# Kernel optimization log

Measured on AMD Instinct MI355X. Metric: run time of the kernel, lower is better.

## Reference

```python
import jax, jax.numpy as jnp
import numpy as np

FS = 512.0
N_PHA = 10
N_AMP = 10
FIR_LEN = 513  # odd, ~1 s at fs=512 -> resolves 2 Hz band edges
N_BINS = 18    # hard-coded in PAC.__init__
TEMP = 0.01    # ModulationIndex temperature (near-hard soft binning)
EPS = 1e-8


def _design_filters():
    # Windowed-sinc FIR bandpass, one kernel per band: h = lp(hi) - lp(lo), Hamming window.
    t = np.arange(FIR_LEN) - (FIR_LEN - 1) / 2.0
    win = np.hamming(FIR_LEN)
    def bp(lo, hi):
        lp = lambda fc: 2.0 * fc / FS * np.sinc(2.0 * fc / FS * t)
        return (lp(hi) - lp(lo)) * win
    pha_c = np.linspace(2.0, 20.0, N_PHA)
    amp_c = np.linspace(60.0, 160.0, N_AMP)
    bands = [(0.75 * c, 1.25 * c) for c in pha_c] + [(0.75 * c, 1.25 * c) for c in amp_c]
    return np.stack([bp(lo, hi) for lo, hi in bands]).astype(np.float32)  # (20, L)


def setup_inputs() -> dict:
    key = jax.random.key(0)
    x = jax.random.normal(key, (4, 16, 4096), dtype=jnp.float32)  # (B, C, T)
    filters = jnp.asarray(_design_filters())                      # (n_pha+n_amp, L)
    return {"x": x, "filters": filters}


def _analytic(sig):
    # FFT-based Hilbert analytic signal along last axis.
    T = sig.shape[-1]
    h = np.zeros(T, np.float32)
    h[0] = 1.0
    if T % 2 == 0:
        h[T // 2] = 1.0
        h[1:T // 2] = 2.0
    else:
        h[1:(T + 1) // 2] = 2.0
    return jnp.fft.ifft(jnp.fft.fft(sig, axis=-1) * jnp.asarray(h), axis=-1)


def reference(x, filters):
    B, C, T = x.shape
    L = filters.shape[-1]
    # Bandpass: (B*C, 1, T) x (n_bands, 1, L) -> (B*C, n_bands, T); symmetric kernels so corr == conv.
    xf = jax.lax.conv_general_dilated(
        x.reshape(-1, 1, T), filters[:, None, :],
        window_strides=(1,), padding=[(L // 2, L // 2)])
    xf = xf.reshape(B, C, -1, T)
    phase = jnp.angle(_analytic(xf[:, :, :N_PHA]))        # (B, C, P, T)
    amplitude = jnp.abs(_analytic(xf[:, :, N_PHA:]))      # (B, C, A, T)
    # Soft circular phase binning (temperature -> near one-hot).
    centers = jnp.asarray((-np.pi + 2.0 * np.pi * (np.arange(N_BINS) + 0.5) / N_BINS).astype(np.float32))
    d = jnp.mod(phase[..., None] - centers + np.pi, 2.0 * np.pi) - np.pi  # (B,C,P,T,K)
    w = jax.nn.softmax(-(d * d) / TEMP, axis=-1)
    # Mean amplitude per phase bin, per (pha, amp) band pair.
    amp_sum = jnp.einsum('bcptk,bcat->bcpak', w, amplitude)  # (B,C,P,A,K)
    cnt = w.sum(axis=-2)                                      # (B,C,P,K)
    mean_amp = amp_sum / (cnt[:, :, :, None, :] + EPS)
    p = mean_amp / (mean_amp.sum(-1, keepdims=True) + EPS)
    log_k = jnp.log(jnp.float32(N_BINS))
    mi = (log_k + (p * jnp.log(p + EPS)).sum(-1)) / log_k    # Tort MI, (B,C,P,A)
    return mi
```

## Files before the change

kernel.cpp:

```cpp
#include <hip/hip_runtime.h>
#include <math.h>

#define T_LEN 4096
#define FIR_L 513
#define N_PHA 10
#define N_AMP 10
#define N_BANDS 20
#define N_BINS 18
#define BC 64

typedef __attribute__((ext_vector_type(8))) short short8;
typedef __attribute__((ext_vector_type(4))) float f32x4;

#define ZA(i) (((i) << 1) + ((((i) >> 4)) << 1))

__device__ float2 twg_dev[1024];

static __device__ __forceinline__ unsigned short f2bf(float x) {
    unsigned u = __float_as_uint(x);
    unsigned r = u + 0x7FFFu + ((u >> 16) & 1u);
    return (unsigned short)(r >> 16);
}

static __device__ __forceinline__ int digitrev12(int p) {
    unsigned rr = __brev((unsigned)p) >> 20;
    rr = ((rr & 0x555u) << 1) | ((rr & 0xAAAu) >> 1);
    return (int)rr;
}

static __device__ __forceinline__ void tw_derive(const float2* tw, int m1,
        float& c1, float& s1, float& c2, float& s2, float& c3, float& s3) {
    const float2 w1 = tw[m1];
    c1 = w1.x; s1 = w1.y;
    s2 = 2.0f * s1 * c1;
    c2 = fmaf(-2.0f * s1, s1, 1.0f);
    c3 = c1 * c2 - s1 * s2;
    s3 = s1 * c2 + c1 * s2;
}

static __device__ __forceinline__ float2 cmul_em(float2 u, float c, float s) {
    return make_float2(u.x * c + u.y * s, u.y * c - u.x * s);
}

static __device__ __forceinline__ void bf_fwd(float2& A, float2& B, float2& C, float2& D,
        float c1, float s1, float c2, float s2, float c3, float s3) {
    const float t0r = A.x + C.x, t0i = A.y + C.y;
    const float t1r = A.x - C.x, t1i = A.y - C.y;
    const float t2r = B.x + D.x, t2i = B.y + D.y;
    const float t3r = B.x - D.x, t3i = B.y - D.y;
    const float y0r = t0r + t2r,  y0i = t0i + t2i;
    const float u1r = t1r + t3i, u1i = t1i - t3r;
    const float u2r = t0r - t2r, u2i = t0i - t2i;
    const float u3r = t1r - t3i, u3i = t1i + t3r;
    A = make_float2(y0r, y0i);
    B = make_float2(u1r * c1 + u1i * s1, u1i * c1 - u1r * s1);
    C = make_float2(u2r * c2 + u2i * s2, u2i * c2 - u2r * s2);
    D = make_float2(u3r * c3 + u3i * s3, u3i * c3 - u3r * s3);
}

static __device__ __forceinline__ void bf_inv(float2& A, float2& B, float2& C, float2& D,
        float c1, float s1, float c2, float s2, float c3, float s3) {
    const float tbr = B.x * c1 - B.y * s1, tbi = B.y * c1 + B.x * s1;
    const float tcr = C.x * c2 - C.y * s2, tci = C.y * c2 + C.x * s2;
    const float tdr = D.x * c3 - D.y * s3, tdi = D.y * c3 + D.x * s3;
    const float ar = A.x, ai = A.y;
    A = make_float2(ar + tbr + tcr + tdr, ai + tbi + tci + tdi);
    B = make_float2(ar - tbi - tcr + tdi, ai + tbr - tci - tdr);
    C = make_float2(ar - tbr + tcr - tdr, ai - tbi + tci - tdi);
    D = make_float2(ar + tbi - tcr - tdi, ai - tbr - tci + tdr);
}

static __device__ __forceinline__ void fft_fwd_passes(float* z, const float2* tw,
                                                      int tid, int s0) {
    for (int s = s0; s < 6; s += 2) {
        const int hl = 10 - 2 * s;
        const int h  = 1 << hl;
        const int h4 = h >> 2;
        const int kk = tid & (h4 - 1);
        const int g  = tid >> (hl - 2);
        const int i0 = (g << (hl + 2)) + kk;
        float2 e[4][4];
#pragma unroll
        for (int j = 0; j < 4; ++j)
#pragma unroll
            for (int r = 0; r < 4; ++r)
                e[j][r] = *(const float2*)&z[ZA(i0 + j * h4 + r * h)];
#pragma unroll
        for (int j = 0; j < 4; ++j) {
            float c1, s1, c2, s2, c3, s3;
            tw_derive(tw, (kk + j * h4) << (2 * s), c1, s1, c2, s2, c3, s3);
            bf_fwd(e[j][0], e[j][1], e[j][2], e[j][3], c1, s1, c2, s2, c3, s3);
        }
        {
            float c1, s1, c2, s2, c3, s3;
            tw_derive(tw, kk << (2 * s + 2), c1, s1, c2, s2, c3, s3);
#pragma unroll
            for (int r = 0; r < 4; ++r)
                bf_fwd(e[0][r], e[1][r], e[2][r], e[3][r], c1, s1, c2, s2, c3, s3);
        }
#pragma unroll
        for (int j = 0; j < 4; ++j)
#pragma unroll
            for (int r = 0; r < 4; ++r)
                *(float2*)&z[ZA(i0 + j * h4 + r * h)] = e[j][r];
        __syncthreads();
    }
}

static __device__ __forceinline__ void fft_fwd_pass1_sparse(
        float* z, const float2* tw, int tid, float2 F, float2 Tl) {
    float c1, s1, c2, s2, c3, s3;
    tw_derive(tw, tid, c1, s1, c2, s2, c3, s3);
    float2 P[4];
    P[0] = F;
    P[1] = cmul_em(F, c1, s1);
    P[2] = cmul_em(F, c2, s2);
    P[3] = cmul_em(F, c3, s3);
    tw_derive(tw, tid + 768, c1, s1, c2, s2, c3, s3);
    const float2 iT  = make_float2(-Tl.y,  Tl.x);
    const float2 nT  = make_float2(-Tl.x, -Tl.y);
    const float2 niT = make_float2( Tl.y, -Tl.x);
    float2 Q[4];
    Q[0] = Tl;
    Q[1] = cmul_em(iT,  c1, s1);
    Q[2] = cmul_em(nT,  c2, s2);
    Q[3] = cmul_em(niT, c3, s3);
    tw_derive(tw, tid << 2, c1, s1, c2, s2, c3, s3);
#pragma unroll
    for (int r = 0; r < 4; ++r) {
        const int ib = tid + (r << 10);
        const float2 A = make_float2(P[r].x + Q[r].x, P[r].y + Q[r].y);
        const float2 B = cmul_em(make_float2(P[r].x - Q[r].y, P[r].y + Q[r].x), c1, s1);
        const float2 C = cmul_em(make_float2(P[r].x - Q[r].x, P[r].y - Q[r].y), c2, s2);
        const float2 D = cmul_em(make_float2(P[r].x + Q[r].y, P[r].y - Q[r].x), c3, s3);
        *(float2*)&z[ZA(ib)]        = A;
        *(float2*)&z[ZA(ib + 256)]  = B;
        *(float2*)&z[ZA(ib + 512)]  = C;
        *(float2*)&z[ZA(ib + 768)]  = D;
    }
}

static __device__ __forceinline__ void fft_inv6(float* z, const float2* tw, int tid) {
#pragma unroll
    for (int s = 0; s < 6; s += 2) {
        const int L  = 1 << (2 * s);
        const int k  = tid & (L - 1);
        const int g  = tid >> (2 * s);
        const int i0 = (g << (2 * s + 4)) + k;
        float2 e[4][4];
#pragma unroll
        for (int j = 0; j < 4; ++j)
#pragma unroll
            for (int r = 0; r < 4; ++r)
                e[j][r] = *(const float2*)&z[ZA(i0 + j * L + (r << (2 * s + 2)))];
        {
            float c1, s1, c2, s2, c3, s3;
            tw_derive(tw, k << (10 - 2 * s), c1, s1, c2, s2, c3, s3);
#pragma unroll
            for (int r = 0; r < 4; ++r)
                bf_inv(e[0][r], e[1][r], e[2][r], e[3][r], c1, s1, c2, s2, c3, s3);
        }
#pragma unroll
        for (int j = 0; j < 4; ++j) {
            float c1, s1, c2, s2, c3, s3;
            tw_derive(tw, (k + j * L) << (8 - 2 * s), c1, s1, c2, s2, c3, s3);
            bf_inv(e[j][0], e[j][1], e[j][2], e[j][3], c1, s1, c2, s2, c3, s3);
        }
#pragma unroll
        for (int j = 0; j < 4; ++j)
#pragma unroll
            for (int r = 0; r < 4; ++r)
                *(float2*)&z[ZA(i0 + j * L + (r << (2 * s + 2)))] = e[j][r];
        __syncthreads();
    }
}

__global__ __launch_bounds__(256) void spectral_pre(
    const float* __restrict__ x,
    const float* __restrict__ filt,
    float2* __restrict__ Xs,
    float2* __restrict__ Hs)
{
    __shared__ float z[8704];
    __shared__ float2 twl[1024];
    __shared__ float fb[FIR_L];

    const int tid = threadIdx.x;
    const int b   = blockIdx.x;

    if (b == BC + N_BANDS) {
        for (int m = tid; m < 1024; m += 256) {
            float ang = (float)m * (6.283185307179586f / 4096.0f);
            float s, c;
            sincosf(ang, &s, &c);
            twg_dev[m] = make_float2(c, s);
        }
        return;
    }

    for (int m = tid; m < 1024; m += 256) {
        float ang = (float)m * (6.283185307179586f / 4096.0f);
        float s, c;
        sincosf(ang, &s, &c);
        twl[m] = make_float2(c, s);
    }

    if (b < BC) {
        const float* xrow = x + b * T_LEN;
        for (int i = tid; i < 4096; i += 256)
            *(float2*)&z[ZA(i)] = make_float2(xrow[i], 0.0f);
    } else {
        const int band = b - BC;
        for (int i = tid; i < FIR_L; i += 256) fb[i] = filt[band * FIR_L + i];
        __syncthreads();
        for (int i = tid; i < 4096; i += 256) {
            float hv = 0.0f;
            if (i < 257)        hv = fb[256 - i];
            else if (i >= 3840) hv = fb[4352 - i];
            *(float2*)&z[ZA(i)] = make_float2(hv, 0.0f);
        }
    }
    __syncthreads();

    fft_fwd_passes(z, twl, tid, 0);

    float2* dst = (b < BC) ? (Xs + b * 4096) : (Hs + (b - BC) * 4096);
    for (int i = tid; i < 4096; i += 256)
        dst[i] = *(const float2*)&z[ZA(i)];
}

__global__ __launch_bounds__(256, 4) void spectral_main(
    const float* __restrict__ x,
    const float* __restrict__ filt,
    const float2* __restrict__ Xs,
    const float2* __restrict__ Hs,
    float* __restrict__ pha,
    unsigned short* __restrict__ amp_bf)
{
    __shared__ float z[8704];
    __shared__ float xe[512];
    __shared__ float fb[FIR_L];

    const int tid  = threadIdx.x;
    const int bc   = blockIdx.x / N_BANDS;
    const int band = blockIdx.x % N_BANDS;
    const float2* tw = twg_dev;

    const float* xrow = x + bc * T_LEN;
    for (int i = tid; i < 512; i += 256)
        xe[i] = (i < 256) ? xrow[i] : xrow[3584 + i];
    for (int i = tid; i < FIR_L; i += 256) fb[i] = filt[band * FIR_L + i];
    __syncthreads();

    float cf = 0.0f, ct = 0.0f;
    for (int l = 0; l <= 255 - tid; ++l)
        cf = fmaf(fb[l], xe[256 + tid + l], cf);
    for (int j = 0; j <= tid; ++j)
        ct = fmaf(fb[512 - tid + j], xe[j], ct);

    fft_fwd_pass1_sparse(z, tw, tid, make_float2(-cf, 0.0f), make_float2(-ct, 0.0f));
    __syncthreads();
    fft_fwd_passes(z, tw, tid, 2);

    const float2* Xrow = Xs + bc * 4096;
    const float2* Hrow = Hs + band * 4096;
    for (int i = tid; i < 4096; i += 256) {
        const float2 X = Xrow[i];
        const float2 H = Hrow[i];
        const float2 C = *(const float2*)&z[ZA(i)];
        float pr = X.x * H.x - X.y * H.y + C.x;
        float pi = X.x * H.y + X.y * H.x + C.y;
        const int f = digitrev12(i);
        const float mf = (f == 0 || f == 2048) ? 1.0f : (f < 2048 ? 2.0f : 0.0f);
        *(float2*)&z[ZA(i)] = make_float2(pr * mf, pi * mf);
    }
    __syncthreads();

    fft_inv6(z, tw, tid);

    const float inv_n = 1.0f / 4096.0f;
    if (band < N_PHA) {
        float* dst = pha + (bc * N_PHA + band) * T_LEN;
        for (int i = tid; i < 4096; i += 256) {
            const float2 zz = *(const float2*)&z[ZA(i)];
            dst[i] = atan2f(zz.y, zz.x);
        }
    } else {
        unsigned short* dst = amp_bf + (bc * N_AMP + (band - N_PHA)) * T_LEN;
        for (int i = tid; i < 4096; i += 256) {
            const float2 zz = *(const float2*)&z[ZA(i)];
            dst[i] = f2bf(sqrtf(zz.x * zz.x + zz.y * zz.y) * inv_n);
        }
    }
}

__global__ __launch_bounds__(512) void bin_mi_mfma(
    const float* __restrict__ pha,
    const unsigned short* __restrict__ amp_bf,
    float* __restrict__ out)
{
    const int tid  = threadIdx.x;
    const int lane = tid & 63;
    const int wv   = tid >> 6;
    const int bc   = blockIdx.x / N_PHA;
    const int p    = blockIdx.x % N_PHA;

    __shared__ unsigned int wbufW[8][18 * 68];
    __shared__ float psum[8][11][N_BINS];
    __shared__ float asum[11][N_BINS];

    const float* phrow = pha + (bc * N_PHA + p) * T_LEN;
    const unsigned short* arow = amp_bf + bc * N_AMP * T_LEN;

    const float PI_F  = 3.14159274101257324f;
    const float INVD  = 2.8647889756541160f;
    const float DELTA = 0.34906585039886590f;
    const float C1    = 12.184696791468343f;
    const float C2    = 69.813170079773180f;

    const int m_ = lane & 15;
    const int q_ = lane >> 4;
    const int n_ = lane & 15;

    short8 zero8;
#pragma unroll
    for (int j = 0; j < 8; ++j) zero8[j] = 0;
    short8 ones8;
#pragma unroll
    for (int j = 0; j < 8; ++j) ones8[j] = (short)0x3F80;

    f32x4 acc0 = {0.f, 0.f, 0.f, 0.f};
    f32x4 acc1 = {0.f, 0.f, 0.f, 0.f};

    const int base_t = wv * 512;
    unsigned short* wh = (unsigned short*)&wbufW[wv][0];

    float2 pp[4];
#pragma unroll
    for (int c = 0; c < 4; ++c)
        pp[c] = *(const float2*)&phrow[base_t + c * 128 + lane * 2];

    for (int chunk = 0; chunk < 4; ++chunk) {
        const int cb = base_t + chunk * 128;

        short8 af[4];
#pragma unroll
        for (int s = 0; s < 4; ++s) {
            const int tA = cb + s * 32 + q_ * 8;
            if (m_ < N_AMP)       af[s] = *(const short8*)(arow + m_ * T_LEN + tA);
            else if (m_ == N_AMP) af[s] = ones8;
            else                  af[s] = zero8;
        }

#pragma unroll
        for (int k = 0; k < N_BINS; ++k)
            wbufW[wv][k * 68 + lane] = 0u;

#pragma unroll
        for (int h = 0; h < 2; ++h) {
            const float ph = h ? pp[chunk].y : pp[chunk].x;
            float u  = (ph + PI_F) * INVD;
            float jf = floorf(u);
            float d  = (u - jf - 0.5f) * DELTA;
            int j0 = (int)jf;
            if (j0 >= N_BINS) j0 -= N_BINS;
            const int jm = (j0 == 0) ? N_BINS - 1 : j0 - 1;
            const int jp = (j0 == N_BINS - 1) ? 0 : j0 + 1;
            const float em = expf(-C1 - C2 * d);
            const float ep = expf(-C1 + C2 * d);
            const float inv = 1.0f / (1.0f + em + ep);
            wh[(j0 * 68 + lane) * 2 + h] = f2bf(inv);
            wh[(jm * 68 + lane) * 2 + h] = f2bf(em * inv);
            wh[(jp * 68 + lane) * 2 + h] = f2bf(ep * inv);
        }
        __builtin_amdgcn_wave_barrier();

#pragma unroll
        for (int s = 0; s < 4; ++s) {
            const int woff = s * 16 + q_ * 4;
            short8 bfrag0 = *(const short8*)&wbufW[wv][n_ * 68 + woff];
            short8 bfrag1 = (n_ < 2)
                ? *(const short8*)&wbufW[wv][(16 + n_) * 68 + woff]
                : zero8;
            acc0 = __builtin_amdgcn_mfma_f32_16x16x32_bf16(af[s], bfrag0, acc0, 0, 0, 0);
            acc1 = __builtin_amdgcn_mfma_f32_16x16x32_bf16(af[s], bfrag1, acc1, 0, 0, 0);
        }
        __builtin_amdgcn_wave_barrier();
    }

#pragma unroll
    for (int r = 0; r < 4; ++r) {
        const int m = q_ * 4 + r;
        if (m < 11) {
            psum[wv][m][n_] = acc0[r];
            if (n_ < 2) psum[wv][m][16 + n_] = acc1[r];
        }
    }
    __syncthreads();

    if (tid < 11 * N_BINS) {
        const int m = tid / N_BINS;
        const int k = tid % N_BINS;
        float s = 0.0f;
#pragma unroll
        for (int w = 0; w < 8; ++w) s += psum[w][m][k];
        asum[m][k] = s;
    }
    __syncthreads();

    if (tid < N_AMP) {
        float ma[N_BINS];
        float msum = 0.0f;
#pragma unroll
        for (int k = 0; k < N_BINS; ++k) {
            float m = asum[tid][k] / (asum[10][k] + 1e-8f);
            ma[k] = m;
            msum += m;
        }
        const float inv = 1.0f / (msum + 1e-8f);
        float acc = 0.0f;
#pragma unroll
        for (int k = 0; k < N_BINS; ++k) {
            float pk = ma[k] * inv;
            acc = fmaf(pk, logf(pk + 1e-8f), acc);
        }
        const float logk = 2.89037175789124f;
        out[(bc * N_PHA + p) * N_AMP + tid] = (logk + acc) / logk;
    }
}

extern "C" void kernel_launch(void* const* d_in, const int* in_sizes, int n_in,
                              void* d_out, int out_size, void* d_ws, size_t ws_size,
                              hipStream_t stream) {
    const float* x    = (const float*)d_in[0];
    const float* filt = (const float*)d_in[1];
    float* out = (float*)d_out;

    float* pha = (float*)d_ws;
    unsigned short* amp_bf = (unsigned short*)(pha + BC * N_PHA * T_LEN);
    float2* Xs = (float2*)(amp_bf + BC * N_AMP * T_LEN);
    float2* Hs = Xs + BC * 4096;

    spectral_pre <<<BC + N_BANDS + 1, 256, 0, stream>>>(x, filt, Xs, Hs);
    spectral_main<<<BC * N_BANDS, 256, 0, stream>>>(x, filt, Xs, Hs, pha, amp_bf);
    bin_mi_mfma  <<<BC * N_PHA,   512, 0, stream>>>(pha, amp_bf, out);
}
```

Baseline: 118.2 us.

## Fuse three kernels into one cooperative persistent kernel with grid syncs

Merges the pre-FFT, spectral main and binning kernels into a single cooperative kernel that loops over work units and separates stages with grid-wide syncs. This removes two kernel launches and their gaps. To fit, the binning stage now runs with 256 threads, so each wave covers twice as many time samples, and the pre stage reads twiddles from global memory instead of a per-block table. The risks are grid sync overhead, a grid capped by occupancy, and less parallelism in the binning stage. Twiddles are written by some blocks and read by others within the same stage before the first grid sync, which may be a race.

```diff
diff --git a/kernel.cpp b/kernel.cpp
--- a/kernel.cpp
+++ b/kernel.cpp
@@ -1,5 +1,8 @@
 #include <hip/hip_runtime.h>
+#include <hip/hip_cooperative_groups.h>
 #include <math.h>
+
+namespace cg = cooperative_groups;
 
 #define T_LEN 4096
 #define FIR_L 513
@@ -175,42 +178,22 @@
     }
 }
 
-__global__ __launch_bounds__(256) void spectral_pre(
-    const float* __restrict__ x,
-    const float* __restrict__ filt,
-    float2* __restrict__ Xs,
-    float2* __restrict__ Hs)
+static __device__ void process_pre_unit(int u,
+        const float* __restrict__ x, const float* __restrict__ filt,
+        float2* __restrict__ Xs, float2* __restrict__ Hs,
+        float* smem_f, int tid)
 {
-    __shared__ float z[8704];
-    __shared__ float2 twl[1024];
-    __shared__ float fb[FIR_L];
-
-    const int tid = threadIdx.x;
-    const int b   = blockIdx.x;
-
-    if (b == BC + N_BANDS) {
-        for (int m = tid; m < 1024; m += 256) {
-            float ang = (float)m * (6.283185307179586f / 4096.0f);
-            float s, c;
-            sincosf(ang, &s, &c);
-            twg_dev[m] = make_float2(c, s);
-        }
-        return;
-    }
-
-    for (int m = tid; m < 1024; m += 256) {
-        float ang = (float)m * (6.283185307179586f / 4096.0f);
-        float s, c;
-        sincosf(ang, &s, &c);
-        twl[m] = make_float2(c, s);
-    }
-
-    if (b < BC) {
-        const float* xrow = x + b * T_LEN;
+    float* z  = smem_f;
+    float* fb = smem_f + 8704;
+
+    __syncthreads();
+
+    if (u < BC) {
+        const float* xrow = x + u * T_LEN;
         for (int i = tid; i < 4096; i += 256)
             *(float2*)&z[ZA(i)] = make_float2(xrow[i], 0.0f);
     } else {
-        const int band = b - BC;
+        const int band = u - BC;
         for (int i = tid; i < FIR_L; i += 256) fb[i] = filt[band * FIR_L + i];
         __syncthreads();
         for (int i = tid; i < 4096; i += 256) {
@@ -222,28 +205,24 @@
     }
     __syncthreads();
 
-    fft_fwd_passes(z, twl, tid, 0);
-
-    float2* dst = (b < BC) ? (Xs + b * 4096) : (Hs + (b - BC) * 4096);
+    fft_fwd_passes(z, twg_dev, tid, 0);
+
+    float2* dst = (u < BC) ? (Xs + u * 4096) : (Hs + (u - BC) * 4096);
     for (int i = tid; i < 4096; i += 256)
         dst[i] = *(const float2*)&z[ZA(i)];
 }
 
-__global__ __launch_bounds__(256, 4) void spectral_main(
-    const float* __restrict__ x,
-    const float* __restrict__ filt,
-    const float2* __restrict__ Xs,
-    const float2* __restrict__ Hs,
-    float* __restrict__ pha,
-    unsigned short* __restrict__ amp_bf)
+static __device__ void process_main_unit(int u,
+        const float* __restrict__ x, const float* __restrict__ filt,
+        const float2* __restrict__ Xs, const float2* __restrict__ Hs,
+        float* __restrict__ pha, unsigned short* __restrict__ amp_bf,
+        float* smem_f, int tid)
 {
-    __shared__ float z[8704];
-    __shared__ float xe[512];
-    __shared__ float fb[FIR_L];
-
-    const int tid  = threadIdx.x;
-    const int bc   = blockIdx.x / N_BANDS;
-    const int band = blockIdx.x % N_BANDS;
+    float* z  = smem_f;
+    float* xe = smem_f + 8704;
+    float* fb = smem_f + 9216;
+    const int bc   = u / N_BANDS;
+    const int band = u % N_BANDS;
     const float2* tw = twg_dev;
 
     const float* xrow = x + bc * T_LEN;
@@ -294,20 +273,18 @@
     }
 }
 
-__global__ __launch_bounds__(512) void bin_mi_mfma(
-    const float* __restrict__ pha,
-    const unsigned short* __restrict__ amp_bf,
-    float* __restrict__ out)
+static __device__ void process_bin_unit(int unit,
+        const float* __restrict__ pha, const unsigned short* __restrict__ amp_bf,
+        float* __restrict__ out, float* smem_f, int tid)
 {
-    const int tid  = threadIdx.x;
+    unsigned int* wbuf = (unsigned int*)smem_f;
+    float* psum = smem_f + 4896;
+    float* asum = smem_f + 5688;
+
     const int lane = tid & 63;
     const int wv   = tid >> 6;
-    const int bc   = blockIdx.x / N_PHA;
-    const int p    = blockIdx.x % N_PHA;
-
-    __shared__ unsigned int wbufW[8][18 * 68];
-    __shared__ float psum[8][11][N_BINS];
-    __shared__ float asum[11][N_BINS];
+    const int bc   = unit / N_PHA;
+    const int p    = unit % N_PHA;
 
     const float* phrow = pha + (bc * N_PHA + p) * T_LEN;
     const unsigned short* arow = amp_bf + bc * N_AMP * T_LEN;
@@ -332,15 +309,16 @@
     f32x4 acc0 = {0.f, 0.f, 0.f, 0.f};
     f32x4 acc1 = {0.f, 0.f, 0.f, 0.f};
 
-    const int base_t = wv * 512;
-    unsigned short* wh = (unsigned short*)&wbufW[wv][0];
-
-    float2 pp[4];
-#pragma unroll
-    for (int c = 0; c < 4; ++c)
+    const int base_t = wv * 1024;
+    unsigned int* wrow = wbuf + wv * 1224;
+    unsigned short* wh = (unsigned short*)wrow;
+
+    float2 pp[8];
+#pragma unroll
+    for (int c = 0; c < 8; ++c)
         pp[c] = *(const float2*)&phrow[base_t + c * 128 + lane * 2];
 
-    for (int chunk = 0; chunk < 4; ++chunk) {
+    for (int chunk = 0; chunk < 8; ++chunk) {
         const int cb = base_t + chunk * 128;
 
         short8 af[4];
@@ -354,7 +332,7 @@
 
 #pragma unroll
         for (int k = 0; k < N_BINS; ++k)
-            wbufW[wv][k * 68 + lane] = 0u;
+            wrow[k * 68 + lane] = 0u;
 
 #pragma unroll
         for (int h = 0; h < 2; ++h) {
@@ -378,9 +356,9 @@
 #pragma unroll
         for (int s = 0; s < 4; ++s) {
             const int woff = s * 16 + q_ * 4;
-            short8 bfrag0 = *(const short8*)&wbufW[wv][n_ * 68 + woff];
+            short8 bfrag0 = *(const short8*)&wrow[n_ * 68 + woff];
             short8 bfrag1 = (n_ < 2)
-                ? *(const short8*)&wbufW[wv][(16 + n_) * 68 + woff]
+                ? *(const short8*)&wrow[(16 + n_) * 68 + woff]
                 : zero8;
             acc0 = __builtin_amdgcn_mfma_f32_16x16x32_bf16(af[s], bfrag0, acc0, 0, 0, 0);
             acc1 = __builtin_amdgcn_mfma_f32_16x16x32_bf16(af[s], bfrag1, acc1, 0, 0, 0);
@@ -392,8 +370,8 @@
     for (int r = 0; r < 4; ++r) {
         const int m = q_ * 4 + r;
         if (m < 11) {
-            psum[wv][m][n_] = acc0[r];
-            if (n_ < 2) psum[wv][m][16 + n_] = acc1[r];
+            psum[(wv * 11 + m) * N_BINS + n_] = acc0[r];
+            if (n_ < 2) psum[(wv * 11 + m) * N_BINS + 16 + n_] = acc1[r];
         }
     }
     __syncthreads();
@@ -401,10 +379,8 @@
     if (tid < 11 * N_BINS) {
         const int m = tid / N_BINS;
         const int k = tid % N_BINS;
-        float s = 0.0f;
-#pragma unroll
-        for (int w = 0; w < 8; ++w) s += psum[w][m][k];
-        asum[m][k] = s;
+        asum[tid] = psum[(0 * 11 + m) * N_BINS + k] + psum[(1 * 11 + m) * N_BINS + k]
+                  + psum[(2 * 11 + m) * N_BINS + k] + psum[(3 * 11 + m) * N_BINS + k];
     }
     __syncthreads();
 
@@ -413,7 +389,7 @@
         float msum = 0.0f;
 #pragma unroll
         for (int k = 0; k < N_BINS; ++k) {
-            float m = asum[tid][k] / (asum[10][k] + 1e-8f);
+            float m = asum[tid * N_BINS + k] / (asum[10 * N_BINS + k] + 1e-8f);
             ma[k] = m;
             msum += m;
         }
@@ -427,6 +403,42 @@
         const float logk = 2.89037175789124f;
         out[(bc * N_PHA + p) * N_AMP + tid] = (logk + acc) / logk;
     }
+}
+
+__global__ __launch_bounds__(256, 4) void pac_fused(
+    const float* __restrict__ x,
+    const float* __restrict__ filt,
+    float2* __restrict__ Xs,
+    float2* __restrict__ Hs,
+    float* __restrict__ pha,
+    unsigned short* __restrict__ amp_bf,
+    float* __restrict__ out)
+{
+    __shared__ __align__(16) float smem_f[9729];
+
+    const int tid = threadIdx.x;
+    const int b   = blockIdx.x;
+    const int nb  = gridDim.x;
+    cg::grid_group gridg = cg::this_grid();
+
+    if (b < BC + N_BANDS) {
+        for (int m = tid; m < 1024; m += 256) {
+            float ang = (float)m * (6.283185307179586f / 4096.0f);
+            float s, c;
+            sincosf(ang, &s, &c);
+            twg_dev[m] = make_float2(c, s);
+        }
+    }
+    for (int u = b; u < BC + N_BANDS; u += nb)
+        process_pre_unit(u, x, filt, Xs, Hs, smem_f, tid);
+    gridg.sync();
+
+    for (int u = b; u < BC * N_BANDS; u += nb)
+        process_main_unit(u, x, filt, Xs, Hs, pha, amp_bf, smem_f, tid);
+    gridg.sync();
+
+    for (int u = b; u < BC * N_PHA; u += nb)
+        process_bin_unit(u, pha, amp_bf, out, smem_f, tid);
 }
 
 extern "C" void kernel_launch(void* const* d_in, const int* in_sizes, int n_in,
@@ -441,7 +453,26 @@
     float2* Xs = (float2*)(amp_bf + BC * N_AMP * T_LEN);
     float2* Hs = Xs + BC * 4096;
 
-    spectral_pre <<<BC + N_BANDS + 1, 256, 0, stream>>>(x, filt, Xs, Hs);
-    spectral_main<<<BC * N_BANDS, 256, 0, stream>>>(x, filt, Xs, Hs, pha, amp_bf);
-    bin_mi_mfma  <<<BC * N_PHA,   512, 0, stream>>>(pha, amp_bf, out);
-}
+    static int grid_blocks = 0;
+    if (grid_blocks == 0) {
+        int dev = 0;
+        hipGetDevice(&dev);
+        hipDeviceProp_t prop;
+        int n_cu = 256;
+        if (hipGetDeviceProperties(&prop, dev) == hipSuccess && prop.multiProcessorCount > 0)
+            n_cu = prop.multiProcessorCount;
+        int nb = 0;
+        hipError_t e = hipOccupancyMaxActiveBlocksPerMultiprocessor(&nb, pac_fused, 256, 0);
+        if (e != hipSuccess || nb < 1) nb = 2;
+        if (nb > 4) nb = 4;
+        long cap  = (long)nb * n_cu;
+        long want = (long)(BC * N_BANDS);
+        grid_blocks = (int)(cap < want ? cap : want);
+        if (grid_blocks < 1) grid_blocks = 1;
+    }
+
+    void* args[] = {(void*)&x, (void*)&filt, (void*)&Xs, (void*)&Hs,
+                    (void*)&pha, (void*)&amp_bf, (void*)&out};
+    hipLaunchCooperativeKernel((const void*)pac_fused, dim3(grid_blocks), dim3(256),
+                               args, 0, stream);
+}
```

After: 284.2 us. 140% more time.

## Precompute wrap-around correction terms in the pre-kernel instead of per-band inline

Applied to the files above, without the earlier changes.

Extra blocks in spectral_pre now compute the circular-convolution edge correction dot products for every (channel, band) pair and write them to a workspace buffer. A new spectral_main_pre then only loads two scalars per thread rather than recomputing the correction from x and the filter. This moves the correction work out of the main spectral kernel and runs it alongside the forward FFTs, at the cost of extra global traffic and a larger pre-kernel grid with unbalanced triangular loops. It falls back to the old inline path when the workspace is too small.

```diff
diff --git a/kernel.cpp b/kernel.cpp
--- a/kernel.cpp
+++ b/kernel.cpp
@@ -179,11 +179,10 @@
     const float* __restrict__ x,
     const float* __restrict__ filt,
     float2* __restrict__ Xs,
-    float2* __restrict__ Hs)
+    float2* __restrict__ Hs,
+    float* __restrict__ corr)
 {
-    __shared__ float z[8704];
-    __shared__ float2 twl[1024];
-    __shared__ float fb[FIR_L];
+    __shared__ __align__(16) float sm[11265];
 
     const int tid = threadIdx.x;
     const int b   = blockIdx.x;
@@ -197,6 +196,51 @@
         }
         return;
     }
+
+    if (b > BC + N_BANDS) {
+        const int cidx = b - (BC + N_BANDS + 1);
+        const int bc   = cidx >> 3;
+        const int oct  = cidx & 7;
+        float* xe  = sm;
+        float* fbs = sm + 512;
+
+        const float* xrow = x + bc * T_LEN;
+        for (int i = tid; i < 512; i += 256)
+            xe[i] = (i < 256) ? xrow[i] : xrow[3584 + i];
+        for (int i = tid; i < N_BANDS * FIR_L; i += 256)
+            fbs[i] = filt[i];
+        __syncthreads();
+
+        const int tl = tid & 31;
+        const int bg = (tid >> 5) & 3;
+        const int t  = oct * 32 + tl;
+        if (tid < 128) {
+#pragma unroll 1
+            for (int b5 = 0; b5 < 5; ++b5) {
+                const int band = bg * 5 + b5;
+                const float* fbp = fbs + band * FIR_L;
+                float cf = 0.0f;
+                for (int l = 0; l <= 255 - t; ++l)
+                    cf = fmaf(fbp[l], xe[256 + t + l], cf);
+                corr[((bc * N_BANDS + band) * 2 + 0) * 256 + t] = cf;
+            }
+        } else {
+#pragma unroll 1
+            for (int b5 = 0; b5 < 5; ++b5) {
+                const int band = bg * 5 + b5;
+                const float* fbp = fbs + band * FIR_L;
+                float ct = 0.0f;
+                for (int j = 0; j <= t; ++j)
+                    ct = fmaf(fbp[512 - t + j], xe[j], ct);
+                corr[((bc * N_BANDS + band) * 2 + 1) * 256 + t] = ct;
+            }
+        }
+        return;
+    }
+
+    float*  z   = sm;
+    float2* twl = (float2*)(sm + 8704);
+    float*  fb  = sm + 8704 + 2048;
 
     for (int m = tid; m < 1024; m += 256) {
         float ang = (float)m * (6.283185307179586f / 4096.0f);
@@ -229,7 +273,60 @@
         dst[i] = *(const float2*)&z[ZA(i)];
 }
 
-__global__ __launch_bounds__(256, 4) void spectral_main(
+__global__ __launch_bounds__(256, 4) void spectral_main_pre(
+    const float* __restrict__ corr,
+    const float2* __restrict__ Xs,
+    const float2* __restrict__ Hs,
+    float* __restrict__ pha,
+    unsigned short* __restrict__ amp_bf)
+{
+    __shared__ __align__(16) float z[8704];
+
+    const int tid  = threadIdx.x;
+    const int bc   = blockIdx.x / N_BANDS;
+    const int band = blockIdx.x % N_BANDS;
+    const float2* tw = twg_dev;
+
+    const float cf = corr[((bc * N_BANDS + band) * 2 + 0) * 256 + tid];
+    const float ct = corr[((bc * N_BANDS + band) * 2 + 1) * 256 + tid];
+
+    fft_fwd_pass1_sparse(z, tw, tid, make_float2(-cf, 0.0f), make_float2(-ct, 0.0f));
+    __syncthreads();
+    fft_fwd_passes(z, tw, tid, 2);
+
+    const float2* Xrow = Xs + bc * 4096;
+    const float2* Hrow = Hs + band * 4096;
+    for (int i = tid; i < 4096; i += 256) {
+        const float2 X = Xrow[i];
+        const float2 H = Hrow[i];
+        const float2 C = *(const float2*)&z[ZA(i)];
+        float pr = X.x * H.x - X.y * H.y + C.x;
+        float pi = X.x * H.y + X.y * H.x + C.y;
+        const int f = digitrev12(i);
+        const float mf = (f == 0 || f == 2048) ? 1.0f : (f < 2048 ? 2.0f : 0.0f);
+        *(float2*)&z[ZA(i)] = make_float2(pr * mf, pi * mf);
+    }
+    __syncthreads();
+
+    fft_inv6(z, tw, tid);
+
+    const float inv_n = 1.0f / 4096.0f;
+    if (band < N_PHA) {
+        float* dst = pha + (bc * N_PHA + band) * T_LEN;
+        for (int i = tid; i < 4096; i += 256) {
+            const float2 zz = *(const float2*)&z[ZA(i)];
+            dst[i] = atan2f(zz.y, zz.x);
+        }
+    } else {
+        unsigned short* dst = amp_bf + (bc * N_AMP + (band - N_PHA)) * T_LEN;
+        for (int i = tid; i < 4096; i += 256) {
+            const float2 zz = *(const float2*)&z[ZA(i)];
+            dst[i] = f2bf(sqrtf(zz.x * zz.x + zz.y * zz.y) * inv_n);
+        }
+    }
+}
+
+__global__ __launch_bounds__(256, 4) void spectral_main_inline(
     const float* __restrict__ x,
     const float* __restrict__ filt,
     const float2* __restrict__ Xs,
@@ -440,8 +537,21 @@
     unsigned short* amp_bf = (unsigned short*)(pha + BC * N_PHA * T_LEN);
     float2* Xs = (float2*)(amp_bf + BC * N_AMP * T_LEN);
     float2* Hs = Xs + BC * 4096;
-
-    spectral_pre <<<BC + N_BANDS + 1, 256, 0, stream>>>(x, filt, Xs, Hs);
-    spectral_main<<<BC * N_BANDS, 256, 0, stream>>>(x, filt, Xs, Hs, pha, amp_bf);
-    bin_mi_mfma  <<<BC * N_PHA,   512, 0, stream>>>(pha, amp_bf, out);
-}
+    float* corr = (float*)(Hs + N_BANDS * 4096);
+
+    const size_t need = (size_t)BC * N_PHA * T_LEN * 4
+                      + (size_t)BC * N_AMP * T_LEN * 2
+                      + (size_t)BC * 4096 * 8
+                      + (size_t)N_BANDS * 4096 * 8
+                      + (size_t)BC * N_BANDS * 2 * 256 * 4;
+    const bool fits = (ws_size >= need);
+
+    if (fits) {
+        spectral_pre<<<BC + N_BANDS + 1 + 512, 256, 0, stream>>>(x, filt, Xs, Hs, corr);
+        spectral_main_pre<<<BC * N_BANDS, 256, 0, stream>>>(corr, Xs, Hs, pha, amp_bf);
+    } else {
+        spectral_pre<<<BC + N_BANDS + 1, 256, 0, stream>>>(x, filt, Xs, Hs, corr);
+        spectral_main_inline<<<BC * N_BANDS, 256, 0, stream>>>(x, filt, Xs, Hs, pha, amp_bf);
+    }
+    bin_mi_mfma<<<BC * N_PHA, 512, 0, stream>>>(pha, amp_bf, out);
+}
```

Result: slower. 121.9 us (+3.1%).
